# Performance work log

Measured on AMD Instinct MI355X. Metric: run time of the kernel, lower is better.

## Reference

```python
import jax, jax.numpy as jnp
import numpy as np

B, T, C = 4, 2048, 1024
NH = 16
HD = C // NH
ROPE_BASE = 10000.0


def setup_inputs() -> dict:
    key = jax.random.key(0)
    k1, k2, k3, k4, k5 = jax.random.split(key, 5)
    s = 1.0 / np.sqrt(C)
    return {
        "x": jax.random.normal(k1, (B, T, C), dtype=jnp.float32),
        "W_qkv": jax.random.normal(k2, (C, 3 * C), dtype=jnp.float32) * s,
        "b_qkv": jax.random.normal(k3, (3 * C,), dtype=jnp.float32) * 0.02,
        "W_proj": jax.random.normal(k4, (C, C), dtype=jnp.float32) * s,
        "b_proj": jax.random.normal(k5, (C,), dtype=jnp.float32) * 0.02,
    }


def _rotate_half(u):
    u1, u2 = u[..., : HD // 2], u[..., HD // 2 :]
    return jnp.concatenate((-u2, u1), axis=-1)


def _rope_cos_sin(t, dtype):
    # inv_freq: [HD/2]; positions: [T]
    inv_freq = 1.0 / (ROPE_BASE ** (jnp.arange(0, HD, 2, dtype=jnp.float32) / HD))
    pos = jnp.arange(t, dtype=jnp.float32)
    freqs = pos[:, None] * inv_freq[None, :]          # [T, HD/2]
    emb = jnp.concatenate((freqs, freqs), axis=-1)    # [T, HD]
    return jnp.cos(emb).astype(dtype), jnp.sin(emb).astype(dtype)


def reference(x, W_qkv, b_qkv, W_proj, b_proj):
    b, t, c = x.shape
    qkv = x @ W_qkv + b_qkv                           # [B,T,3C]
    q, k, v = jnp.split(qkv, 3, axis=-1)
    # [B,T,C] -> [B,NH,T,HD]
    def to_heads(u):
        return u.reshape(b, t, NH, HD).transpose(0, 2, 1, 3)
    q, k, v = to_heads(q), to_heads(k), to_heads(v)
    cos, sin = _rope_cos_sin(t, x.dtype)              # [T,HD] each; broadcast over B,NH
    q = q * cos + _rotate_half(q) * sin
    k = k * cos + _rotate_half(k) * sin
    att = jnp.einsum("bhqd,bhkd->bhqk", q, k) * (1.0 / np.sqrt(HD))
    causal = jnp.tril(jnp.ones((t, t), dtype=bool))
    att = jnp.where(causal, att, -jnp.inf)
    att = jax.nn.softmax(att, axis=-1)
    y = jnp.einsum("bhqk,bhkd->bhqd", att, v)         # [B,NH,T,HD]
    y = y.transpose(0, 2, 1, 3).reshape(b, t, c)
    return y @ W_proj + b_proj
```

## Files before the change

### kernel.cpp

```cpp
#include <hip/hip_runtime.h>
#include <cstdint>
#include <cstddef>

typedef __attribute__((ext_vector_type(8))) short short8;
typedef __attribute__((ext_vector_type(4))) float float4x;
typedef __attribute__((ext_vector_type(16))) float float16x;
typedef __attribute__((ext_vector_type(2))) unsigned int uint2v;

__device__ __forceinline__ uint16_t f2b(float f){
  uint32_t u = __builtin_bit_cast(uint32_t, f);
  u += 0x7FFFu + ((u >> 16) & 1u);
  return (uint16_t)(u >> 16);
}
__device__ __forceinline__ float b2f(uint16_t h){
  uint32_t u = ((uint32_t)h) << 16;
  return __builtin_bit_cast(float, u);
}
__device__ __forceinline__ float4x zero4(){
  float4x v; v[0]=0.f; v[1]=0.f; v[2]=0.f; v[3]=0.f; return v;
}
__device__ __forceinline__ float16x zero16(){
  float16x v;
#pragma unroll
  for (int i = 0; i < 16; i++) v[i] = 0.f;
  return v;
}
__device__ __forceinline__ uint32_t cvtpk(float lo, float hi){
  uint32_t r;
  asm("v_cvt_pk_bf16_f32 %0, %1, %2" : "=v"(r) : "v"(lo), "v"(hi));
  return r;
}
__device__ __forceinline__ void plswap(uint32_t &a, uint32_t &b){
#if __has_builtin(__builtin_amdgcn_permlane32_swap)
  uint2v r = __builtin_amdgcn_permlane32_swap(a, b, false, false);
  a = r[0]; b = r[1];
#else
  uint32_t a2 = (uint32_t)__shfl_xor((int)a, 32, 64);
  uint32_t b2 = (uint32_t)__shfl_xor((int)b, 32, 64);
  bool lo = ((threadIdx.x & 63) < 32);
  uint32_t an = lo ? a : b2;
  uint32_t bn = lo ? a2 : b;
  a = an; b = bn;
#endif
}
__device__ __forceinline__ float fexp2(float x){
#if __has_builtin(__builtin_amdgcn_exp2f)
  return __builtin_amdgcn_exp2f(x);
#else
  return exp2f(x);
#endif
}
__device__ __forceinline__ void gload16(const uint16_t* g, uint16_t* l){
  __builtin_amdgcn_global_load_lds(
      (const __attribute__((address_space(1))) uint32_t*)g,
      (__attribute__((address_space(3))) uint32_t*)l, 16, 0, 0);
}

__global__ __launch_bounds__(256) void k_f32_to_bf16(const float* __restrict__ in,
                                                     uint16_t* __restrict__ out, int n4){
  int i = blockIdx.x * 256 + threadIdx.x;
  if (i < n4){
    float4 v = ((const float4*)in)[i];
    ushort4 o;
    o.x = f2b(v.x); o.y = f2b(v.y); o.z = f2b(v.z); o.w = f2b(v.w);
    ((ushort4*)out)[i] = o;
  }
}

__global__ __launch_bounds__(256) void k_transpose_bf16(const float* __restrict__ W,
                                                        uint16_t* __restrict__ Wt, int K, int N){
  __shared__ float tile[32][33];
  int k0 = blockIdx.y * 32, n0 = blockIdx.x * 32;
  int c = threadIdx.x & 31, r0 = threadIdx.x >> 5;
  for (int rr = r0; rr < 32; rr += 8)
    tile[rr][c] = W[(size_t)(k0 + rr) * N + n0 + c];
  __syncthreads();
  for (int rr = r0; rr < 32; rr += 8)
    Wt[(size_t)(n0 + rr) * K + k0 + c] = f2b(tile[c][rr]);
}

__global__ __launch_bounds__(512) void k_gemm_qkv(const uint16_t* __restrict__ A,
                                                  const uint16_t* __restrict__ Bt,
                                                  const float* __restrict__ bias,
                                                  uint16_t* __restrict__ qkv,
                                                  uint16_t* __restrict__ vt){
  __shared__ __align__(16) uint16_t SM[49152];
  const int tid = threadIdx.x, lane = tid & 63, wave = tid >> 6;
  const int wm = wave >> 2, wn = wave & 3;
  const int quad = lane >> 4, l15 = lane & 15;

  const int wg = (blockIdx.x & 7) * 96 + (blockIdx.x >> 3);
  const int by = wg / 12, bx = wg % 12;
  const int m0 = by * 128, n0 = bx * 256;

  const int rsr = tid >> 2;
  const int cg  = (tid & 3) ^ ((tid >> 3) & 3);
  const size_t aRow  = (size_t)(m0 + rsr)       * 1024 + cg * 8;
  const size_t bRow0 = (size_t)(n0 + rsr)       * 1024 + cg * 8;
  const size_t bRow1 = (size_t)(n0 + rsr + 128) * 1024 + cg * 8;
  const int dA = tid * 8, dB0 = tid * 8, dB1 = 4096 + tid * 8;
  const int mc8 = (quad ^ ((l15 >> 1) & 3)) * 8;

  float4x acc[4][4];
#pragma unroll
  for (int i = 0; i < 4; i++)
#pragma unroll
    for (int j = 0; j < 4; j++) acc[i][j] = zero4();

#define STAGE(H) { \
  const int sl_ = (H) & 3; \
  gload16(A  + aRow  + (size_t)(H)*32, &SM[sl_*4096 + dA]); \
  gload16(Bt + bRow0 + (size_t)(H)*32, &SM[16384 + sl_*8192 + dB0]); \
  gload16(Bt + bRow1 + (size_t)(H)*32, &SM[16384 + sl_*8192 + dB1]); }
#define LOADFRAGS(SL) \
  short8 af[4], bf[4]; \
  bf[0] = *(const short8*)&SM[16384 + (SL)*8192 + (wn*64 +  0 + l15)*32 + mc8]; \
  bf[1] = *(const short8*)&SM[16384 + (SL)*8192 + (wn*64 + 16 + l15)*32 + mc8]; \
  bf[2] = *(const short8*)&SM[16384 + (SL)*8192 + (wn*64 + 32 + l15)*32 + mc8]; \
  bf[3] = *(const short8*)&SM[16384 + (SL)*8192 + (wn*64 + 48 + l15)*32 + mc8]; \
  af[0] = *(const short8*)&SM[(SL)*4096 + (wm*64 +  0 + l15)*32 + mc8]; \
  af[1] = *(const short8*)&SM[(SL)*4096 + (wm*64 + 16 + l15)*32 + mc8]; \
  af[2] = *(const short8*)&SM[(SL)*4096 + (wm*64 + 32 + l15)*32 + mc8]; \
  af[3] = *(const short8*)&SM[(SL)*4096 + (wm*64 + 48 + l15)*32 + mc8];
#define MM() { \
  __builtin_amdgcn_s_setprio(1); \
  _Pragma("unroll") \
  for (int mt_ = 0; mt_ < 4; mt_++){ \
    acc[mt_][0] = __builtin_amdgcn_mfma_f32_16x16x32_bf16(af[mt_], bf[0], acc[mt_][0], 0, 0, 0); \
    acc[mt_][1] = __builtin_amdgcn_mfma_f32_16x16x32_bf16(af[mt_], bf[1], acc[mt_][1], 0, 0, 0); \
    acc[mt_][2] = __builtin_amdgcn_mfma_f32_16x16x32_bf16(af[mt_], bf[2], acc[mt_][2], 0, 0, 0); \
    acc[mt_][3] = __builtin_amdgcn_mfma_f32_16x16x32_bf16(af[mt_], bf[3], acc[mt_][3], 0, 0, 0); \
  } \
  __builtin_amdgcn_s_setprio(0); }
#define BAR() \
  __builtin_amdgcn_sched_barrier(0); __builtin_amdgcn_s_barrier(); __builtin_amdgcn_sched_barrier(0);

  STAGE(0) STAGE(1) STAGE(2)
  asm volatile("s_waitcnt vmcnt(6)" ::: "memory");
  BAR();

  for (int p = 0; p < 29; ++p){
    const int sl = p & 3;
    LOADFRAGS(sl)
    STAGE(p + 3)
    MM()
    asm volatile("s_waitcnt vmcnt(6)" ::: "memory");
    BAR();
  }
  {
    LOADFRAGS(1)
    MM()
    asm volatile("s_waitcnt vmcnt(3)" ::: "memory");
    BAR();
  }
  {
    LOADFRAGS(2)
    MM()
    asm volatile("s_waitcnt vmcnt(0)" ::: "memory");
    BAR();
  }
  {
    LOADFRAGS(3)
    MM()
  }
#undef STAGE
#undef LOADFRAGS
#undef MM
#undef BAR

  if (bx < 8){
#pragma unroll
    for (int mt = 0; mt < 4; mt++){
      int grow = m0 + wm*64 + mt*16 + quad*4;
      int tpos = grow & 2047;
#pragma unroll
      for (int nt = 0; nt < 2; nt++){
        int gcol = n0 + wn*64 + nt*16 + l15;
        float bv1 = bias[gcol], bv2 = bias[gcol + 32];
        int i = nt*16 + l15;
        float inv = exp2f(-(float)i * 0.4152410118609203f);
#pragma unroll
        for (int r = 0; r < 4; r++){
          float ang = (float)(tpos + r) * inv;
          float s, c;
          __sincosf(ang, &s, &c);
          float u1 = acc[mt][nt][r]   + bv1;
          float u2 = acc[mt][nt+2][r] + bv2;
          qkv[(size_t)(grow + r)*3072 + gcol]      = f2b(u1*c - u2*s);
          qkv[(size_t)(grow + r)*3072 + gcol + 32] = f2b(u2*c + u1*s);
        }
      }
    }
  } else {
    const int h = (bx - 8)*4 + wn;
    const int bb = m0 >> 11;
    const int tb0 = (m0 & 2047) + wm*64;
    const int bh64 = (bb*16 + h)*64;
    uint16_t* T = &SM[wave*4608];
    const int d32 = lane & 31, th = lane >> 5;
    __syncthreads();
#pragma unroll
    for (int nt = 0; nt < 4; nt++){
      int gcol = n0 + wn*64 + nt*16 + l15;
      float bv = bias[gcol];
#pragma unroll
      for (int mt = 0; mt < 4; mt++)
#pragma unroll
        for (int r = 0; r < 4; r++)
          T[(nt*16 + l15)*72 + mt*16 + quad*4 + r] = f2b(acc[mt][nt][r] + bv);
    }
    __syncthreads();
#pragma unroll
    for (int dd = 0; dd < 2; dd++)
#pragma unroll
      for (int it = 0; it < 4; it++){
        short8 v = *(const short8*)&T[(d32 + 32*dd)*72 + th*32 + it*8];
        *(short8*)&vt[((size_t)(bh64 + d32 + 32*dd))*2048 + tb0 + th*32 + it*8] = v;
      }
  }
}

__global__ __launch_bounds__(256, 3) void k_gemm_proj(const uint16_t* __restrict__ A,
                                                      const uint16_t* __restrict__ Bt,
                                                      const float* __restrict__ bias,
                                                      float* __restrict__ Cout,
                                                      int M, int N, int K){
  __shared__ __align__(16) uint16_t As[2][128*32];
  __shared__ __align__(16) uint16_t Bs[2][128*32];
  const int tid = threadIdx.x, lane = tid & 63, wave = tid >> 6;
  const int wr = wave >> 1, wc = wave & 1;
  const int m0 = blockIdx.y * 128, n0 = blockIdx.x * 128;
  const int quad = lane >> 4, l15 = lane & 15;
  const int rowA = tid >> 2, chA = tid & 3;

  float4x acc[4][4];
  for (int i = 0; i < 4; i++) for (int j = 0; j < 4; j++) acc[i][j] = zero4();

  const uint16_t* pa0 = &A[(size_t)(m0 + rowA)*K + chA*8];
  const uint16_t* pa1 = &A[(size_t)(m0 + rowA + 64)*K + chA*8];
  const uint16_t* pb0 = &Bt[(size_t)(n0 + rowA)*K + chA*8];
  const uint16_t* pb1 = &Bt[(size_t)(n0 + rowA + 64)*K + chA*8];

  gload16(pa0, &As[0][tid*8]);
  gload16(pa1, &As[0][64*32 + tid*8]);
  gload16(pb0, &Bs[0][tid*8]);
  gload16(pb1, &Bs[0][64*32 + tid*8]);

  int buf = 0;
  for (int k0 = 0; k0 < K; k0 += 32){
    __syncthreads();
    if (k0 + 32 < K){
      int nb = buf ^ 1;
      gload16(pa0 + k0 + 32, &As[nb][tid*8]);
      gload16(pa1 + k0 + 32, &As[nb][64*32 + tid*8]);
      gload16(pb0 + k0 + 32, &Bs[nb][tid*8]);
      gload16(pb1 + k0 + 32, &Bs[nb][64*32 + tid*8]);
    }
    short8 af[4], bfr[4];
#pragma unroll
    for (int mt = 0; mt < 4; mt++)
      af[mt] = *(const short8*)&As[buf][(wr*64 + mt*16 + l15)*32 + quad*8];
#pragma unroll
    for (int nt = 0; nt < 4; nt++)
      bfr[nt] = *(const short8*)&Bs[buf][(wc*64 + nt*16 + l15)*32 + quad*8];
#pragma unroll
    for (int mt = 0; mt < 4; mt++)
#pragma unroll
      for (int nt = 0; nt < 4; nt++)
        acc[mt][nt] = __builtin_amdgcn_mfma_f32_16x16x32_bf16(af[mt], bfr[nt], acc[mt][nt], 0, 0, 0);
    buf ^= 1;
  }

#pragma unroll
  for (int mt = 0; mt < 4; mt++){
    int grow = m0 + wr*64 + mt*16 + quad*4;
#pragma unroll
    for (int nt = 0; nt < 4; nt++){
      int gcol = n0 + wc*64 + nt*16 + l15;
      float bv = bias[gcol];
#pragma unroll
      for (int r = 0; r < 4; r++)
        Cout[(size_t)(grow + r)*N + gcol] = acc[mt][nt][r] + bv;
    }
  }
}

__global__ __launch_bounds__(512) void k_attn(const uint16_t* __restrict__ qkv,
                                              const uint16_t* __restrict__ vt,
                                              uint16_t* __restrict__ y){
  __shared__ __align__(16) uint16_t Klds[2][64*64];
  __shared__ __align__(16) uint16_t Vlds[2][64*64];

  const int Did = blockIdx.x;
  const int g = Did & 7, ii = Did >> 3;
  const int bh = g*8 + (ii >> 2);
  const int X  = ii & 3;
  const int b = bh >> 4, h = bh & 15;
  const int lane = threadIdx.x & 63, w = threadIdx.x >> 6;
  const int l31 = lane & 31, hi = lane >> 5;

  const uint16_t* Qbase  = qkv + (size_t)b*2048*3072 + h*64;
  const uint16_t* Kbase  = qkv + (size_t)b*2048*3072 + 1024 + h*64;
  const uint16_t* Vtbase = vt  + (size_t)bh*64*2048;

  const float S2 = 0.18033688011112042f;
  const float M2 = 43.28085122666890f;

  const int isV  = w >> 2;
  const int rbase = (w & 3) * 16;
  const int rsub = lane >> 3, csub = lane & 7;

  const int cA = X, cB = 7 - X;
  const int KT_A = 4*cA + 4;
  const int TS = 36;

  int c = cA;
  int qr = c*256 + w*32;

  short8 aq[4];
#pragma unroll
  for (int kc = 0; kc < 4; kc++)
    aq[kc] = *(const short8*)&Qbase[(size_t)(qr + l31)*3072 + kc*16 + hi*8];

  float16x o[2];
  o[0] = zero16(); o[1] = zero16();
  float lr4[4] = {0.f, 0.f, 0.f, 0.f};

  auto epilogue = [&](){
    float l = (lr4[0] + lr4[1]) + (lr4[2] + lr4[3]);
    l += __shfl_xor(l, 32, 64);
    float linv = 1.f / l;
    float lv[16];
#pragma unroll
    for (int r = 0; r < 16; r++)
      lv[r] = __shfl(linv, (r&3) + 8*(r>>2) + 4*hi, 64);
#pragma unroll
    for (int dt = 0; dt < 2; dt++)
#pragma unroll
      for (int r = 0; r < 16; r++){
        int row = (r&3) + 8*(r>>2) + 4*hi;
        y[((size_t)(b*2048 + qr + row))*1024 + h*64 + dt*32 + l31] = f2b(o[dt][r] * lv[r]);
      }
  };

#pragma unroll
  for (int j = 0; j < 2; j++){
    int r  = rbase + j*8 + rsub;
    int cg = csub ^ (r & 7);
    if (isV) gload16(Vtbase + (size_t)r*2048 + cg*8, &Vlds[0][(rbase + j*8)*64 + lane*8]);
    else     gload16(Kbase  + (size_t)r*3072 + cg*8, &Klds[0][(rbase + j*8)*64 + lane*8]);
  }

  int cur = 0;
  for (int t = 0; t < TS; ++t){
    __syncthreads();
    const int kt = (t < KT_A) ? t : t - KT_A;
    if (t + 1 < TS){
      const int ktn = (t + 1 < KT_A) ? t + 1 : t + 1 - KT_A;
      int nb = cur ^ 1;
#pragma unroll
      for (int j = 0; j < 2; j++){
        int r  = rbase + j*8 + rsub;
        int cg = csub ^ (r & 7);
        if (isV) gload16(Vtbase + (size_t)r*2048 + (size_t)ktn*64 + cg*8,
                         &Vlds[nb][(rbase + j*8)*64 + lane*8]);
        else     gload16(Kbase  + (size_t)(ktn*64 + r)*3072 + cg*8,
                         &Klds[nb][(rbase + j*8)*64 + lane*8]);
      }
    }

    if (t == KT_A){
      epilogue();
      c = cB; qr = c*256 + w*32;
#pragma unroll
      for (int kc = 0; kc < 4; kc++)
        aq[kc] = *(const short8*)&Qbase[(size_t)(qr + l31)*3072 + kc*16 + hi*8];
      o[0] = zero16(); o[1] = zero16();
      lr4[0] = lr4[1] = lr4[2] = lr4[3] = 0.f;
    }

    if (kt*64 <= qr + 31){
      float16x p0 = zero16(), p1 = zero16();
      __builtin_amdgcn_s_setprio(1);
#pragma unroll
      for (int kc = 0; kc < 4; kc++){
        const int ch = 2*kc + hi;
        short8 ak0 = *(const short8*)&Klds[cur][(l31)*64      + ((ch ^ (l31 & 7))*8)];
        short8 ak1 = *(const short8*)&Klds[cur][(32 + l31)*64 + ((ch ^ (l31 & 7))*8)];
        p0 = __builtin_amdgcn_mfma_f32_32x32x16_bf16(ak0, aq[kc], p0, 0, 0, 0);
        p1 = __builtin_amdgcn_mfma_f32_32x32x16_bf16(ak1, aq[kc], p1, 0, 0, 0);
      }
      __builtin_amdgcn_s_setprio(0);

      if (kt*64 + 63 > qr){
        const int tq = qr + l31;
#pragma unroll
        for (int r = 0; r < 16; r++){
          int kb = kt*64 + (r&3) + 8*(r>>2) + 4*hi;
          if (kb > tq)      p0[r] = -1e30f;
          if (kb + 32 > tq) p1[r] = -1e30f;
        }
      }

#pragma unroll
      for (int r = 0; r < 16; r++){
        float e0 = fexp2(__builtin_fmaf(p0[r], S2, -M2));
        float e1 = fexp2(__builtin_fmaf(p1[r], S2, -M2));
        lr4[r & 3] += e0 + e1;
        p0[r] = e0; p1[r] = e1;
      }

      __builtin_amdgcn_s_setprio(1);
#pragma unroll
      for (int kc = 0; kc < 4; kc++){
        const int e8 = (kc & 1)*8;
        uint32_t w0, w1, w2, w3;
        if (kc < 2){
          w0 = cvtpk(p0[e8+0], p0[e8+1]); w1 = cvtpk(p0[e8+2], p0[e8+3]);
          w2 = cvtpk(p0[e8+4], p0[e8+5]); w3 = cvtpk(p0[e8+6], p0[e8+7]);
        } else {
          w0 = cvtpk(p1[e8+0], p1[e8+1]); w1 = cvtpk(p1[e8+2], p1[e8+3]);
          w2 = cvtpk(p1[e8+4], p1[e8+5]); w3 = cvtpk(p1[e8+6], p1[e8+7]);
        }
        plswap(w0, w2);
        plswap(w1, w3);
        union { uint32_t u[4]; short8 s; } ap;
        ap.u[0] = w0; ap.u[1] = w1; ap.u[2] = w2; ap.u[3] = w3;

        const int ch = 2*kc + hi;
        short8 bv0 = *(const short8*)&Vlds[cur][(l31)*64      + ((ch ^ (l31 & 7))*8)];
        short8 bv1 = *(const short8*)&Vlds[cur][(32 + l31)*64 + ((ch ^ (l31 & 7))*8)];
        o[0] = __builtin_amdgcn_mfma_f32_32x32x16_bf16(ap.s, bv0, o[0], 0, 0, 0);
        o[1] = __builtin_amdgcn_mfma_f32_32x32x16_bf16(ap.s, bv1, o[1], 0, 0, 0);
      }
      __builtin_amdgcn_s_setprio(0);
    }
    cur ^= 1;
  }

  epilogue();
}

extern "C" void kernel_launch(void* const* d_in, const int* in_sizes, int n_in,
                              void* d_out, int out_size, void* d_ws, size_t ws_size,
                              hipStream_t stream){
  const float* x     = (const float*)d_in[0];
  const float* Wqkv  = (const float*)d_in[1];
  const float* bqkv  = (const float*)d_in[2];
  const float* Wproj = (const float*)d_in[3];
  const float* bproj = (const float*)d_in[4];

  uint16_t* p = (uint16_t*)d_ws;
  uint16_t* xb    = p; p += (size_t)8192*1024;
  uint16_t* wqkvt = p; p += (size_t)3072*1024;
  uint16_t* wprjt = p; p += (size_t)1024*1024;
  uint16_t* qkv   = p; p += (size_t)8192*3072;
  uint16_t* vt    = p; p += (size_t)64*64*2048;
  uint16_t* yb    = p; p += (size_t)8192*1024;

  k_f32_to_bf16<<<8192, 256, 0, stream>>>(x, xb, 2097152);
  k_transpose_bf16<<<dim3(96, 32), 256, 0, stream>>>(Wqkv, wqkvt, 1024, 3072);
  k_transpose_bf16<<<dim3(32, 32), 256, 0, stream>>>(Wproj, wprjt, 1024, 1024);
  k_gemm_qkv<<<768, 512, 0, stream>>>(xb, wqkvt, bqkv, qkv, vt);
  k_attn<<<256, 512, 0, stream>>>(qkv, vt, yb);
  k_gemm_proj<<<dim3(8, 64), 256, 0, stream>>>(yb, wprjt, bproj, (float*)d_out, 8192, 1024, 1024);
}
```

Measured before the change: 259.2 us.

## Triple-buffer attention K/V loads and merge prep kernels into one launch

The attention kernel moves from a double-buffered K/V LDS ring to a three-slot ring that prefetches two tiles ahead. It waits on partial vmcnt counts with raw s_barrier instead of a full __syncthreads, so global-to-LDS loads overlap more compute. Separately, the x conversion and both weight transposes become a single launch with the work picked by block index, saving two launches. The cost is 16KB more LDS per block and hand-tuned waitcnt logic that is fragile to get right.

```diff
diff --git a/kernel.cpp b/kernel.cpp
--- a/kernel.cpp
+++ b/kernel.cpp
@@ -56,21 +56,24 @@
       (__attribute__((address_space(3))) uint32_t*)l, 16, 0, 0);
 }
 
-__global__ __launch_bounds__(256) void k_f32_to_bf16(const float* __restrict__ in,
-                                                     uint16_t* __restrict__ out, int n4){
-  int i = blockIdx.x * 256 + threadIdx.x;
-  if (i < n4){
-    float4 v = ((const float4*)in)[i];
+__global__ __launch_bounds__(256) void k_prep(const float* __restrict__ x, uint16_t* __restrict__ xb,
+                                              const float* __restrict__ Wqkv, uint16_t* __restrict__ wqkvt,
+                                              const float* __restrict__ Wproj, uint16_t* __restrict__ wprjt){
+  __shared__ float tile[32][33];
+  const int bid = blockIdx.x;
+  if (bid < 8192){
+    int i = bid * 256 + threadIdx.x;
+    float4 v = ((const float4*)x)[i];
     ushort4 o;
     o.x = f2b(v.x); o.y = f2b(v.y); o.z = f2b(v.z); o.w = f2b(v.w);
-    ((ushort4*)out)[i] = o;
-  }
-}
-
-__global__ __launch_bounds__(256) void k_transpose_bf16(const float* __restrict__ W,
-                                                        uint16_t* __restrict__ Wt, int K, int N){
-  __shared__ float tile[32][33];
-  int k0 = blockIdx.y * 32, n0 = blockIdx.x * 32;
+    ((ushort4*)xb)[i] = o;
+    return;
+  }
+  const float* W; uint16_t* Wt; int N, i;
+  if (bid < 8192 + 3072){ W = Wqkv;  Wt = wqkvt; N = 3072; i = bid - 8192; }
+  else                  { W = Wproj; Wt = wprjt; N = 1024; i = bid - 8192 - 3072; }
+  const int K = 1024, nb = N >> 5;
+  int k0 = (i / nb) * 32, n0 = (i % nb) * 32;
   int c = threadIdx.x & 31, r0 = threadIdx.x >> 5;
   for (int rr = r0; rr < 32; rr += 8)
     tile[rr][c] = W[(size_t)(k0 + rr) * N + n0 + c];
@@ -288,8 +291,8 @@
 __global__ __launch_bounds__(512) void k_attn(const uint16_t* __restrict__ qkv,
                                               const uint16_t* __restrict__ vt,
                                               uint16_t* __restrict__ y){
-  __shared__ __align__(16) uint16_t Klds[2][64*64];
-  __shared__ __align__(16) uint16_t Vlds[2][64*64];
+  __shared__ __align__(16) uint16_t Klds[3][64*64];
+  __shared__ __align__(16) uint16_t Vlds[3][64*64];
 
   const int Did = blockIdx.x;
   const int g = Did & 7, ii = Did >> 3;
@@ -343,31 +346,28 @@
       }
   };
 
-#pragma unroll
-  for (int j = 0; j < 2; j++){
-    int r  = rbase + j*8 + rsub;
-    int cg = csub ^ (r & 7);
-    if (isV) gload16(Vtbase + (size_t)r*2048 + cg*8, &Vlds[0][(rbase + j*8)*64 + lane*8]);
-    else     gload16(Kbase  + (size_t)r*3072 + cg*8, &Klds[0][(rbase + j*8)*64 + lane*8]);
-  }
-
-  int cur = 0;
+#define STAGE_KV(TT, SL) { \
+  const int kt_ = ((TT) < KT_A) ? (TT) : (TT) - KT_A; \
+  _Pragma("unroll") \
+  for (int j = 0; j < 2; j++){ \
+    int r_  = rbase + j*8 + rsub; \
+    int cg_ = csub ^ (r_ & 7); \
+    if (isV) gload16(Vtbase + (size_t)r_*2048 + (size_t)kt_*64 + cg_*8, \
+                     &Vlds[SL][(rbase + j*8)*64 + lane*8]); \
+    else     gload16(Kbase  + (size_t)(kt_*64 + r_)*3072 + cg_*8, \
+                     &Klds[SL][(rbase + j*8)*64 + lane*8]); \
+  } }
+#define ABAR() \
+  __builtin_amdgcn_sched_barrier(0); __builtin_amdgcn_s_barrier(); __builtin_amdgcn_sched_barrier(0);
+
+  STAGE_KV(0, 0)
+  STAGE_KV(1, 1)
+  asm volatile("s_waitcnt vmcnt(2)" ::: "memory");
+  ABAR();
+
   for (int t = 0; t < TS; ++t){
-    __syncthreads();
-    const int kt = (t < KT_A) ? t : t - KT_A;
-    if (t + 1 < TS){
-      const int ktn = (t + 1 < KT_A) ? t + 1 : t + 1 - KT_A;
-      int nb = cur ^ 1;
-#pragma unroll
-      for (int j = 0; j < 2; j++){
-        int r  = rbase + j*8 + rsub;
-        int cg = csub ^ (r & 7);
-        if (isV) gload16(Vtbase + (size_t)r*2048 + (size_t)ktn*64 + cg*8,
-                         &Vlds[nb][(rbase + j*8)*64 + lane*8]);
-        else     gload16(Kbase  + (size_t)(ktn*64 + r)*3072 + cg*8,
-                         &Klds[nb][(rbase + j*8)*64 + lane*8]);
-      }
-    }
+    const int sl = t % 3;
+    if (t + 2 < TS) STAGE_KV(t + 2, (t + 2) % 3)
 
     if (t == KT_A){
       epilogue();
@@ -379,14 +379,15 @@
       lr4[0] = lr4[1] = lr4[2] = lr4[3] = 0.f;
     }
 
+    const int kt = (t < KT_A) ? t : t - KT_A;
     if (kt*64 <= qr + 31){
       float16x p0 = zero16(), p1 = zero16();
       __builtin_amdgcn_s_setprio(1);
 #pragma unroll
       for (int kc = 0; kc < 4; kc++){
         const int ch = 2*kc + hi;
-        short8 ak0 = *(const short8*)&Klds[cur][(l31)*64      + ((ch ^ (l31 & 7))*8)];
-        short8 ak1 = *(const short8*)&Klds[cur][(32 + l31)*64 + ((ch ^ (l31 & 7))*8)];
+        short8 ak0 = *(const short8*)&Klds[sl][(l31)*64      + ((ch ^ (l31 & 7))*8)];
+        short8 ak1 = *(const short8*)&Klds[sl][(32 + l31)*64 + ((ch ^ (l31 & 7))*8)];
         p0 = __builtin_amdgcn_mfma_f32_32x32x16_bf16(ak0, aq[kc], p0, 0, 0, 0);
         p1 = __builtin_amdgcn_mfma_f32_32x32x16_bf16(ak1, aq[kc], p1, 0, 0, 0);
       }
@@ -428,15 +429,20 @@
         ap.u[0] = w0; ap.u[1] = w1; ap.u[2] = w2; ap.u[3] = w3;
 
         const int ch = 2*kc + hi;
-        short8 bv0 = *(const short8*)&Vlds[cur][(l31)*64      + ((ch ^ (l31 & 7))*8)];
-        short8 bv1 = *(const short8*)&Vlds[cur][(32 + l31)*64 + ((ch ^ (l31 & 7))*8)];
+        short8 bv0 = *(const short8*)&Vlds[sl][(l31)*64      + ((ch ^ (l31 & 7))*8)];
+        short8 bv1 = *(const short8*)&Vlds[sl][(32 + l31)*64 + ((ch ^ (l31 & 7))*8)];
         o[0] = __builtin_amdgcn_mfma_f32_32x32x16_bf16(ap.s, bv0, o[0], 0, 0, 0);
         o[1] = __builtin_amdgcn_mfma_f32_32x32x16_bf16(ap.s, bv1, o[1], 0, 0, 0);
       }
       __builtin_amdgcn_s_setprio(0);
     }
-    cur ^= 1;
-  }
+
+    if (t < TS - 2) asm volatile("s_waitcnt vmcnt(2)" ::: "memory");
+    else            asm volatile("s_waitcnt vmcnt(0)" ::: "memory");
+    ABAR();
+  }
+#undef STAGE_KV
+#undef ABAR
 
   epilogue();
 }
@@ -458,9 +464,7 @@
   uint16_t* vt    = p; p += (size_t)64*64*2048;
   uint16_t* yb    = p; p += (size_t)8192*1024;
 
-  k_f32_to_bf16<<<8192, 256, 0, stream>>>(x, xb, 2097152);
-  k_transpose_bf16<<<dim3(96, 32), 256, 0, stream>>>(Wqkv, wqkvt, 1024, 3072);
-  k_transpose_bf16<<<dim3(32, 32), 256, 0, stream>>>(Wproj, wprjt, 1024, 1024);
+  k_prep<<<12288, 256, 0, stream>>>(x, xb, Wqkv, wqkvt, Wproj, wprjt);
   k_gemm_qkv<<<768, 512, 0, stream>>>(xb, wqkvt, bqkv, qkv, vt);
   k_attn<<<256, 512, 0, stream>>>(qkv, vt, yb);
   k_gemm_proj<<<dim3(8, 64), 256, 0, stream>>>(yb, wprjt, bproj, (float*)d_out, 8192, 1024, 1024);
```

Measured after the change: 253.2 us. -2.3%, faster.
